# Optimization experiments

Measured on AMD Instinct MI355X. Metric: run time of the kernel, lower is better.

Reference implementation:

```python
import jax, jax.numpy as jnp
import numpy as np

SAMPLE_RATE = 44100
LOWEST_HZ = 55.0
L_ORDER = 5
NUM_COEFF = L_ORDER + 1          # 6 loop-filter coefficients
NUM_ACTIVE = NUM_COEFF + 1       # 7 taps for linear interpolation
VEC_SIZE = int(SAMPLE_RATE // LOWEST_HZ) + NUM_ACTIVE  # 808 = LPC order
N_FRAMES = 128
N_SAMPLES = 65536


def _natural_cubic_spline(y, t_out):
    """Natural cubic spline through y[n, d] at uniform knots on [0,1], eval at t_out[T]."""
    n, d = y.shape
    h = 1.0 / (n - 1)
    # second derivatives M with natural BC (M0 = Mn-1 = 0): tridiag solve
    rhs = 6.0 * (y[2:] - 2.0 * y[1:-1] + y[:-2]) / (h * h)          # [n-2, d]
    T = 4.0 * jnp.eye(n - 2, dtype=y.dtype) \
        + jnp.eye(n - 2, k=1, dtype=y.dtype) + jnp.eye(n - 2, k=-1, dtype=y.dtype)
    M_inner = jnp.linalg.solve(T, rhs)
    zero = jnp.zeros((1, d), y.dtype)
    M = jnp.concatenate([zero, M_inner, zero], axis=0)              # [n, d]
    idx = jnp.clip(jnp.floor(t_out * (n - 1)).astype(jnp.int32), 0, n - 2)
    s = (t_out - idx.astype(y.dtype) * h)[:, None]                  # [T, 1]
    yi, yi1, Mi, Mi1 = y[idx], y[idx + 1], M[idx], M[idx + 1]
    b = (yi1 - yi) / h - h * (2.0 * Mi + Mi1) / 6.0
    return yi + b * s + 0.5 * Mi * s * s + (Mi1 - Mi) * (s ** 3) / (6.0 * h)


def setup_inputs() -> dict:
    key = jax.random.key(0)
    k1, k2, k3 = jax.random.split(key, 3)
    # delay in samples, in [100, 300) so floor(delay)+6 < VEC_SIZE always
    delay_len_frames = 100.0 + 200.0 * jax.random.uniform(k1, (N_FRAMES,), dtype=jnp.float32)
    raw_gain = jnp.zeros((), jnp.float32)  # nn.Parameter init 0.0
    # raw (pre-sigmoid) coefficients, uniform in coeff_range = (-2, 0)
    raw_coeff_frames = jax.random.uniform(k2, (N_FRAMES, NUM_COEFF), dtype=jnp.float32,
                                          minval=-2.0, maxval=0.0)
    exc_coefficients = jnp.zeros((1, N_SAMPLES, 1), jnp.float32)  # zeros init, order 1
    burst = jax.random.normal(k3, (N_SAMPLES,), jnp.float32)      # excitation noise burst
    return {"delay_len_frames": delay_len_frames, "raw_gain": raw_gain,
            "raw_coeff_frames": raw_coeff_frames, "exc_coefficients": exc_coefficients,
            "burst": burst, "n_samples": N_SAMPLES}


def _forward(delay_len_frames, raw_gain, raw_coeff_frames, exc_coefficients, burst, n_samples):
    dtype = jnp.float32
    # get_constrained_coefficients: sigmoid -> normalize to sum 1 -> scale by gain
    sig = jax.nn.sigmoid(raw_coeff_frames)
    coeff_frames = sig / sig.sum(-1, keepdims=True) * jax.nn.sigmoid(raw_gain)  # [F, 6]
    # get_upsampled_parameters: natural cubic spline from n_frames -> n_samples
    t_out = jnp.linspace(0.0, 1.0, n_samples, dtype=dtype)
    delay_i = _natural_cubic_spline(delay_len_frames[:, None].astype(dtype), t_out)[:, 0]  # [T]
    b = _natural_cubic_spline(coeff_frames.astype(dtype), t_out)                           # [T, 6]
    # linear fractional-delay taps: z_l..z_l+6 (floor->int breaks grad, alfa keeps it)
    z_l = jnp.floor(delay_i).astype(jnp.int32)
    alfa = (delay_i - z_l.astype(dtype))[:, None]
    # A[t, z_l+i] values (sparse representation of the [T, VEC_SIZE] tap matrix)
    vals = -jnp.concatenate([(1.0 - alfa) * b[:, :1],
                             alfa * b[:, :-1] + (1.0 - alfa) * b[:, 1:],
                             alfa * b[:, -1:]], axis=1)                                    # [T, 7]
    # excitation LPC (order 1, time-varying): x[t] = burst[t] - a[t]*x[t-1]
    a1 = exc_coefficients[0, :, 0]
    def exc_step(ym1, inp):
        xt, at = inp
        y = xt - at * ym1
        return y, y
    _, x = jax.lax.scan(exc_step, jnp.zeros((), dtype), (burst.astype(dtype), a1))
    # Karplus-Strong recursion: y[t] = x[t] - sum_j A[t,j]*y[t-1-j]; buf[j] = y[t-1-j]
    def ks_step(buf, inp):
        xt, v, z = inp
        taps = jax.lax.dynamic_slice(buf, (z,), (NUM_ACTIVE,))
        y = xt - jnp.dot(v, taps)
        buf = jnp.concatenate([y[None], buf[:-1]])
        return buf, y
    buf0 = jnp.zeros((VEC_SIZE,), dtype)
    _, y_out = jax.lax.scan(ks_step, buf0, (x, vals, z_l))
    return y_out


def reference(delay_len_frames, raw_gain, raw_coeff_frames, exc_coefficients, burst, n_samples):
    return _forward(delay_len_frames, raw_gain, raw_coeff_frames,
                    exc_coefficients, burst, n_samples)
```

## Files before the change

### kernel.cpp

```cpp
#include <hip/hip_runtime.h>
#include <math.h>
#include <limits.h>

#define N_SAMPLES 65536
#define N_FRAMES  128
#define NUM_COEFF 6
#define NSEG      126
#define VEC_SIZE  808
#define ZCLAMP    (VEC_SIZE - 7)

#define WS_XL    0
#define WS_PP    262144
#define WS_VALS  524288
#define WS_TM    2621440
#define WS_TC    2621696
#define WS_D     2621952
#define WS_PL    2622464
#define WS_MQ    5768192

__global__ __launch_bounds__(256) void k_front(
    const float* __restrict__ delay_len,
    const float* __restrict__ raw_gain,
    const float* __restrict__ raw_coeff,
    const float* __restrict__ exc,
    const float* __restrict__ burst,
    float* __restrict__ ws)
{
    const int tid = threadIdx.x;
    const int b = blockIdx.x;

    if (b >= 256) {
        float* xl = ws + WS_XL / 4;
        float* PP = ws + WS_PP / 4;
        float* TM = ws + WS_TM / 4;
        float* TC = ws + WS_TC / 4;
        const int tile = b - 256;
        const int base = tile * 1024 + tid * 4;

        if (tile == 0 && tid == 0) *(int*)((char*)ws + WS_D) = 0x7fffffff;

        const float4 a4 = *(const float4*)(exc + base);
        const float4 b4 = *(const float4*)(burst + base);

        float m = -a4.x,            c = b4.x;
        m = -a4.y * m;              c = b4.y - a4.y * c;
        m = -a4.z * m;              c = b4.z - a4.z * c;
        m = -a4.w * m;              c = b4.w - a4.w * c;

        __shared__ float sm[256], sc[256];
        sm[tid] = m; sc[tid] = c;
        __syncthreads();
        for (int off = 1; off < 256; off <<= 1) {
            const float cm = sm[tid], cc = sc[tid];
            float pm = 1.f, pc = 0.f;
            if (tid >= off) { pm = sm[tid - off]; pc = sc[tid - off]; }
            __syncthreads();
            if (tid >= off) { sm[tid] = cm * pm; sc[tid] = cm * pc + cc; }
            __syncthreads();
        }
        float y = (tid == 0) ? 0.f : sc[tid - 1];
        float P = (tid == 0) ? 1.f : sm[tid - 1];

        float4 x4, p4;
        y = b4.x - a4.x * y;  P = -a4.x * P;  x4.x = y; p4.x = P;
        y = b4.y - a4.y * y;  P = -a4.y * P;  x4.y = y; p4.y = P;
        y = b4.z - a4.z * y;  P = -a4.z * P;  x4.z = y; p4.z = P;
        y = b4.w - a4.w * y;  P = -a4.w * P;  x4.w = y; p4.w = P;

        *(float4*)(xl + base) = x4;
        *(float4*)(PP + base) = p4;
        if (tid == 255) { TM[tile] = sm[255]; TC[tile] = sc[255]; }
        return;
    }

    float* vals8 = ws + WS_VALS / 4;
    __shared__ float Y[7][N_FRAMES];
    __shared__ float M[7][N_FRAMES];
    __shared__ double cp[NSEG];
    __shared__ double dp[7][NSEG];

    if (tid < N_FRAMES) {
        float s[NUM_COEFF];
        float sum = 0.f;
        for (int j = 0; j < NUM_COEFF; ++j) {
            s[j] = 1.f / (1.f + expf(-raw_coeff[tid * NUM_COEFF + j]));
            sum += s[j];
        }
        const float gain = 1.f / (1.f + expf(-raw_gain[0]));
        for (int j = 0; j < NUM_COEFF; ++j)
            Y[1 + j][tid] = s[j] / sum * gain;
        Y[0][tid] = delay_len[tid];
    }
    __syncthreads();

    if (tid == 0) {
        cp[0] = 0.25;
        for (int i = 1; i < NSEG; ++i) cp[i] = 1.0 / (4.0 - cp[i - 1]);
    }
    __syncthreads();

    if (tid < 7) {
        const float* y = Y[tid];
        const double inv_h2 = 127.0 * 127.0;
        double prev = 6.0 * ((double)y[2] - 2.0 * (double)y[1] + (double)y[0]) * inv_h2 * 0.25;
        dp[tid][0] = prev;
        for (int i = 1; i < NSEG; ++i) {
            double ri = 6.0 * ((double)y[i + 2] - 2.0 * (double)y[i + 1] + (double)y[i]) * inv_h2;
            prev = (ri - prev) * cp[i];
            dp[tid][i] = prev;
        }
        float* Mc = M[tid];
        Mc[0] = 0.f; Mc[N_FRAMES - 1] = 0.f;
        double mi = dp[tid][NSEG - 1];
        Mc[NSEG] = (float)mi;
        for (int i = NSEG - 2; i >= 0; --i) {
            mi = dp[tid][i] - cp[i] * mi;
            Mc[i + 1] = (float)mi;
        }
    }
    __syncthreads();

    const int t = b * 256 + tid;
    const float h = 1.0f / 127.0f;
    const float tf = (float)t * (1.0f / 65535.0f);
    int idx = (int)floorf(tf * 127.0f);
    idx = min(max(idx, 0), 126);
    const float s = tf - (float)idx * h;
    const float s2 = s * s;
    const float s3 = s2 * s;

    float o[7];
#pragma unroll
    for (int c = 0; c < 7; ++c) {
        const float yi  = Y[c][idx];
        const float yi1 = Y[c][idx + 1];
        const float Mi  = M[c][idx];
        const float Mi1 = M[c][idx + 1];
        const float bb = (yi1 - yi) / h - h * (2.f * Mi + Mi1) / 6.f;
        o[c] = yi + bb * s + 0.5f * Mi * s2 + (Mi1 - Mi) * s3 / (6.f * h);
    }
    const float delay = o[0];
    int z = (int)floorf(delay);
    const float alfa = delay - (float)z;
    z = min(max(z, 0), ZCLAMP);

    float v[8];
    v[0] = -((1.f - alfa) * o[1]);
#pragma unroll
    for (int j = 1; j <= 5; ++j)
        v[j] = -(alfa * o[j] + (1.f - alfa) * o[j + 1]);
    v[6] = -(alfa * o[6]);
    v[7] = (float)z;

    float4* vp = (float4*)(vals8 + (size_t)t * 8);
    vp[0] = make_float4(v[0], v[1], v[2], v[3]);
    vp[1] = make_float4(v[4], v[5], v[6], v[7]);
}

__device__ __forceinline__ unsigned int bf16_hi(float f) {
    unsigned int b = __float_as_uint(f);
    b = b + 0x7fffu + ((b >> 16) & 1u);
    return b & 0xffff0000u;
}
__device__ __forceinline__ unsigned int bf16_lo(float f) {
    unsigned int b = __float_as_uint(f);
    b = b + 0x7fffu + ((b >> 16) & 1u);
    return b >> 16;
}

__global__ __launch_bounds__(256) void k_exp(float* __restrict__ ws)
{
    __shared__ float accL[256 * 33];
    __shared__ float xwin[1920];
    __shared__ float yin[64];
    __shared__ int dmin;
    const int tid = threadIdx.x;
    const int T0 = blockIdx.x * 256;
    const int t = T0 + tid;
    const int wlo = T0 - 1664;

    const float* xl = ws + WS_XL / 4;
    const float* PP = ws + WS_PP / 4;
    const float* vals8 = ws + WS_VALS / 4;
    const float* TM = ws + WS_TM / 4;
    const float* TC = ws + WS_TC / 4;
    float4* PL = (float4*)((char*)ws + WS_PL);
    float4* MQ = (float4*)((char*)ws + WS_MQ);
    int* D = (int*)((char*)ws + WS_D);

    float* acc = accL + tid * 33;
#pragma unroll
    for (int o = 0; o < 32; ++o) acc[o] = 0.f;

    if (tid == 0) {
        dmin = 0x7fffffff;
        float y = 0.f;
        for (int k = 0; k < 64; ++k) {
            yin[k] = y;
            y = TC[k] + TM[k] * y;
        }
    }
    __syncthreads();

    for (int i = tid; i < 1920; i += 256) {
        const int p = wlo + i;
        float xv = 0.f;
        if (p >= 0 && p < N_SAMPLES)
            xv = xl[p] + PP[p] * yin[p >> 10];
        xwin[i] = xv;
    }
    __syncthreads();

#define XREAD(p) xwin[(p) - wlo]

    const float4* vp = (const float4*)(vals8 + (size_t)t * 8);
    const float4 r0 = vp[0], r1 = vp[1];
    const float vj[7] = {r0.x, r0.y, r0.z, r0.w, r1.x, r1.y, r1.z};
    const int m0 = t - 1 - (int)r1.w;
    float X1 = XREAD(t);

    float4 s0[7], s1[7];
    float xs[7];
    int sm0[7];
    bool val[7];
    int pmin = INT_MAX;
#pragma unroll
    for (int j = 0; j < 7; ++j) {
        const int s = m0 - j;
        val[j] = (s >= 0);
        const int si = val[j] ? s : 0;
        const float4* sp = (const float4*)(vals8 + (size_t)si * 8);
        s0[j] = sp[0]; s1[j] = sp[1];
        xs[j] = XREAD(val[j] ? s : t);
        sm0[j] = s - 1 - (int)s1[j].w;
        if (val[j]) pmin = min(pmin, sm0[j]);
    }
    if (pmin == INT_MAX) pmin = t - 900;
    const int B1 = (pmin - 6) & ~3;

#pragma unroll
    for (int j = 0; j < 7; ++j) {
        if (!val[j]) continue;
        X1 -= vj[j] * xs[j];
        const float sv[7] = {s0[j].x, s0[j].y, s0[j].z, s0[j].w,
                             s1[j].x, s1[j].y, s1[j].z};
        const int ob = sm0[j] - B1;
#pragma unroll
        for (int k = 0; k < 7; ++k) {
            int o = ob - k;
            o = min(max(o, 0), 31);
            acc[o] += vj[j] * sv[k];
        }
    }

    float c1f[32];
#pragma unroll
    for (int o = 0; o < 32; ++o) { c1f[o] = acc[o]; acc[o] = 0.f; }

    float X15 = X1;
    int first = -1;
#pragma unroll
    for (int o = 0; o < 32; ++o)
        if (first < 0 && c1f[o] != 0.f && (B1 + o) >= 0) first = o;

    int B2 = 0, maxq = INT_MIN;
    if (first >= 0) {
        const int pf = B1 + first;
        const float zf = ((const float4*)(vals8 + (size_t)pf * 8))[1].w;
        B2 = ((pf - 1 - (int)zf) - 6) & ~3;

#pragma unroll
        for (int o = 0; o < 32; ++o) {
            const float co = c1f[o];
            const int p = B1 + o;
            if (co == 0.f || p < 0) continue;
            const float4* pv = (const float4*)(vals8 + (size_t)p * 8);
            const float4 v0 = pv[0], v1 = pv[1];
            X15 += co * XREAD(p);
            const int rp = p - 1 - (int)v1.w;
            maxq = max(maxq, rp);
            const float sv[7] = {v0.x, v0.y, v0.z, v0.w, v1.x, v1.y, v1.z};
            const int ob = rp - B2;
#pragma unroll
            for (int j = 0; j < 7; ++j) {
                int oo = ob - j;
                oo = min(max(oo, 0), 27);
                acc[oo] -= co * sv[j];
            }
        }
    }
#undef XREAD

    unsigned int u[14];
#pragma unroll
    for (int i = 0; i < 14; ++i)
        u[i] = bf16_lo(acc[2 * i]) | (bf16_lo(acc[2 * i + 1]) << 16);

    PL[t]             = make_float4(__uint_as_float(u[0]),  __uint_as_float(u[1]),
                                    __uint_as_float(u[2]),  __uint_as_float(u[3]));
    PL[t + 65536]     = make_float4(__uint_as_float(u[4]),  __uint_as_float(u[5]),
                                    __uint_as_float(u[6]),  __uint_as_float(u[7]));
    PL[t + 2 * 65536] = make_float4(__uint_as_float(u[8]),  __uint_as_float(u[9]),
                                    __uint_as_float(u[10]), __uint_as_float(u[11]));
    MQ[t] = make_float4(X15, (float)(B2 & 2047),
                        __uint_as_float(u[12]), __uint_as_float(u[13]));

    if (first >= 0 && maxq > INT_MIN) atomicMin(&dmin, t - maxq);
    __syncthreads();
    if (tid == 0) atomicMin(D, dmin);
}

__device__ __forceinline__ void bar_lgkm() {
    asm volatile("s_waitcnt lgkmcnt(0)\n\ts_barrier" ::: "memory");
}

typedef float f32x4 __attribute__((ext_vector_type(4)));

#define GLD4(dst, p)                                                           \
    asm volatile("global_load_dwordx4 %0, %1, off" : "=v"(dst) : "v"(p))

#define VWAIT8(a, b, c, d)                                                     \
    asm volatile("s_waitcnt vmcnt(8)"                                          \
        : "+v"(a), "+v"(b), "+v"(c), "+v"(d))

#define DOT2BF(acc_, a_, b_)                                                   \
    asm("v_dot2_f32_bf16 %0, %1, %2, %0" : "+v"(acc_) : "v"(a_), "v"(b_))

__global__ __launch_bounds__(512, 1) void k_ks3(
    const float* __restrict__ ws_c,
    float* __restrict__ out)
{
    __shared__ __align__(16) unsigned short ringb[4096];
    const int tid = threadIdx.x;
    const f32x4* PL = (const f32x4*)((const char*)ws_c + WS_PL);
    const f32x4* MQ = (const f32x4*)((const char*)ws_c + WS_MQ);
    const int* Dp = (const int*)((const char*)ws_c + WS_D);

    for (int i = tid; i < 4096; i += 512) ringb[i] = 0;
    __syncthreads();

    int C = *Dp;
    if (C > 512) C = 512;
    if (C < 1) C = 1;
    const int C3 = 3 * C;

#define PRE(P0, P1, P2, PM, BASE)                                              \
    do {                                                                       \
        int tL = (BASE) + tid; if (tL > N_SAMPLES - 1) tL = N_SAMPLES - 1;     \
        GLD4(P0, PL + tL);             GLD4(P1, PL + tL + 65536);              \
        GLD4(P2, PL + tL + 2 * 65536); GLD4(PM, MQ + tL);                      \
    } while (0)

#define DOT(P0, P1, P2, PM, YOUT)                                              \
    do {                                                                       \
        const int idx_ = (int)(PM).y;                                          \
        const unsigned int u_[14] = {                                          \
            __float_as_uint((P0).x), __float_as_uint((P0).y),                  \
            __float_as_uint((P0).z), __float_as_uint((P0).w),                  \
            __float_as_uint((P1).x), __float_as_uint((P1).y),                  \
            __float_as_uint((P1).z), __float_as_uint((P1).w),                  \
            __float_as_uint((P2).x), __float_as_uint((P2).y),                  \
            __float_as_uint((P2).z), __float_as_uint((P2).w),                  \
            __float_as_uint((PM).z), __float_as_uint((PM).w)};                 \
        float p0 = 0.f, p1 = 0.f;                                              \
        _Pragma("unroll")                                                      \
        for (int q = 0; q < 7; ++q) {                                          \
            const uint2 rr_ = *(const uint2*)&ringb[idx_ + 4 * q];             \
            DOT2BF(p0, u_[2 * q],     rr_.x);                                  \
            DOT2BF(p1, u_[2 * q + 1], rr_.y);                                  \
        }                                                                      \
        YOUT = (PM).x + (p0 + p1);                                             \
    } while (0)

#define STEP(P0, P1, P2, PM, S_)                                               \
    do {                                                                       \
        VWAIT8(P0, P1, P2, PM);                                                \
        const int t0 = (S_) + tid;                                             \
        if (tid < C && t0 < N_SAMPLES) {                                       \
            float y0; DOT(P0, P1, P2, PM, y0);                                 \
            const int w = t0 & 2047;                                           \
            const unsigned short yb = (unsigned short)bf16_lo(y0);             \
            ringb[w] = yb; ringb[w + 2048] = yb; out[t0] = y0;                 \
        }                                                                      \
        PRE(P0, P1, P2, PM, (S_) + C3);                                        \
        bar_lgkm();                                                            \
    } while (0)

    f32x4 A0, A1, A2, AM;
    f32x4 B0, B1, B2, BM;
    f32x4 U0, U1, U2, UM;

    PRE(A0, A1, A2, AM, 0);
    PRE(B0, B1, B2, BM, C);
    PRE(U0, U1, U2, UM, 2 * C);
    for (int S = 0; S < N_SAMPLES; S += C3) {
        STEP(A0, A1, A2, AM, S);
        STEP(B0, B1, B2, BM, S + C);
        STEP(U0, U1, U2, UM, S + 2 * C);
    }
#undef STEP
#undef DOT
#undef PRE
}

extern "C" void kernel_launch(void* const* d_in, const int* in_sizes, int n_in,
                              void* d_out, int out_size, void* d_ws, size_t ws_size,
                              hipStream_t stream)
{
    const float* delay_len = (const float*)d_in[0];
    const float* raw_gain  = (const float*)d_in[1];
    const float* raw_coeff = (const float*)d_in[2];
    const float* exc       = (const float*)d_in[3];
    const float* burst     = (const float*)d_in[4];
    float* ws  = (float*)d_ws;
    float* out = (float*)d_out;

    hipLaunchKernelGGL(k_front, dim3(320), dim3(256), 0, stream,
                       delay_len, raw_gain, raw_coeff, exc, burst, ws);
    hipLaunchKernelGGL(k_exp, dim3(256), dim3(256), 0, stream, ws);
    hipLaunchKernelGGL(k_ks3, dim3(1), dim3(512), 0, stream, ws, out);
}
```

Baseline: 188.4 us.

## Precompute spline pivots at compile time, parallel-scan carries, shrink KS block

The tridiagonal pivot table is now computed at compile time into constant memory, which removes a serial loop and a barrier from the front kernel. The 64-tile carry chain in the expansion kernel becomes a wavefront shuffle scan instead of a serial loop run by one thread. The single-block Karplus-Strong kernel drops from 512 to 320 threads and caps the chunk size C at 320, which may reduce barrier cost per step but processes fewer samples per chunk.

```diff
diff --git a/kernel.cpp b/kernel.cpp
--- a/kernel.cpp
+++ b/kernel.cpp
@@ -17,6 +17,15 @@
 #define WS_D     2621952
 #define WS_PL    2622464
 #define WS_MQ    5768192
+
+struct CpTab { double v[NSEG]; };
+static constexpr CpTab make_cp() {
+    CpTab t{};
+    t.v[0] = 0.25;
+    for (int i = 1; i < NSEG; ++i) t.v[i] = 1.0 / (4.0 - t.v[i - 1]);
+    return t;
+}
+__device__ __constant__ CpTab CP = make_cp();
 
 __global__ __launch_bounds__(256) void k_front(
     const float* __restrict__ delay_len,
@@ -76,7 +85,6 @@
     float* vals8 = ws + WS_VALS / 4;
     __shared__ float Y[7][N_FRAMES];
     __shared__ float M[7][N_FRAMES];
-    __shared__ double cp[NSEG];
     __shared__ double dp[7][NSEG];
 
     if (tid < N_FRAMES) {
@@ -90,12 +98,6 @@
         for (int j = 0; j < NUM_COEFF; ++j)
             Y[1 + j][tid] = s[j] / sum * gain;
         Y[0][tid] = delay_len[tid];
-    }
-    __syncthreads();
-
-    if (tid == 0) {
-        cp[0] = 0.25;
-        for (int i = 1; i < NSEG; ++i) cp[i] = 1.0 / (4.0 - cp[i - 1]);
     }
     __syncthreads();
 
@@ -106,7 +108,7 @@
         dp[tid][0] = prev;
         for (int i = 1; i < NSEG; ++i) {
             double ri = 6.0 * ((double)y[i + 2] - 2.0 * (double)y[i + 1] + (double)y[i]) * inv_h2;
-            prev = (ri - prev) * cp[i];
+            prev = (ri - prev) * CP.v[i];
             dp[tid][i] = prev;
         }
         float* Mc = M[tid];
@@ -114,7 +116,7 @@
         double mi = dp[tid][NSEG - 1];
         Mc[NSEG] = (float)mi;
         for (int i = NSEG - 2; i >= 0; --i) {
-            mi = dp[tid][i] - cp[i] * mi;
+            mi = dp[tid][i] - CP.v[i] * mi;
             Mc[i + 1] = (float)mi;
         }
     }
@@ -192,13 +194,17 @@
 #pragma unroll
     for (int o = 0; o < 32; ++o) acc[o] = 0.f;
 
-    if (tid == 0) {
-        dmin = 0x7fffffff;
-        float y = 0.f;
-        for (int k = 0; k < 64; ++k) {
-            yin[k] = y;
-            y = TC[k] + TM[k] * y;
-        }
+    if (tid == 0) dmin = 0x7fffffff;
+    if (tid < 64) {
+        float m = TM[tid], c = TC[tid];
+#pragma unroll
+        for (int off = 1; off < 64; off <<= 1) {
+            const float pm = __shfl_up(m, off, 64);
+            const float pc = __shfl_up(c, off, 64);
+            if (tid >= off) { c = fmaf(m, pc, c); m *= pm; }
+        }
+        const float yp = __shfl_up(c, 1, 64);
+        yin[tid] = (tid == 0) ? 0.f : yp;
     }
     __syncthreads();
 
@@ -326,7 +332,7 @@
 #define DOT2BF(acc_, a_, b_)                                                   \
     asm("v_dot2_f32_bf16 %0, %1, %2, %0" : "+v"(acc_) : "v"(a_), "v"(b_))
 
-__global__ __launch_bounds__(512, 1) void k_ks3(
+__global__ __launch_bounds__(320, 1) void k_ks3(
     const float* __restrict__ ws_c,
     float* __restrict__ out)
 {
@@ -336,11 +342,11 @@
     const f32x4* MQ = (const f32x4*)((const char*)ws_c + WS_MQ);
     const int* Dp = (const int*)((const char*)ws_c + WS_D);
 
-    for (int i = tid; i < 4096; i += 512) ringb[i] = 0;
+    for (int i = tid; i < 4096; i += 320) ringb[i] = 0;
     __syncthreads();
 
     int C = *Dp;
-    if (C > 512) C = 512;
+    if (C > 320) C = 320;
     if (C < 1) C = 1;
     const int C3 = 3 * C;
 
@@ -418,5 +424,5 @@
     hipLaunchKernelGGL(k_front, dim3(320), dim3(256), 0, stream,
                        delay_len, raw_gain, raw_coeff, exc, burst, ws);
     hipLaunchKernelGGL(k_exp, dim3(256), dim3(256), 0, stream, ws);
-    hipLaunchKernelGGL(k_ks3, dim3(1), dim3(512), 0, stream, ws, out);
-}
+    hipLaunchKernelGGL(k_ks3, dim3(1), dim3(320), 0, stream, ws, out);
+}
```

Measured after the change: 162.5 us. 13.7% less time.
